# Kernel optimization log

Hardware: AMD Instinct MI355X
Metric: run time of the kernel (lower is better)

## Reference

```python
import jax, jax.numpy as jnp
import numpy as np

N_NODES = 100000
N_EDGES = 1600000
D_IN = 128
D_OUT = 128


def setup_inputs() -> dict:
    key = jax.random.key(0)
    k1, k2, k3 = jax.random.split(key, 3)
    x = jax.random.normal(k1, (N_NODES, D_IN), dtype=jnp.float32)
    edge_index = jax.random.randint(k2, (2, N_EDGES), 0, N_NODES, dtype=jnp.int64)
    # glorot-style init for the lazily-created weight
    scale = jnp.sqrt(6.0 / (D_IN + D_OUT)).astype(jnp.float32)
    weight = jax.random.uniform(k3, (D_IN, D_OUT), dtype=jnp.float32, minval=-1.0, maxval=1.0) * scale
    bias = jnp.zeros((D_OUT,), dtype=jnp.float32)
    return {"x": x, "edge_index": edge_index, "weight": weight, "bias": bias}


def reference(x, edge_index, weight, bias):
    N = x.shape[0]
    row, col = edge_index[0], edge_index[1]
    # add_remaining_self_loops: drop existing self-loops (equivalently zero their
    # weight) and append a self-loop of weight 1.0 for every node (improved=False).
    ew = jnp.where(row == col, 0.0, 1.0).astype(x.dtype)
    loop = jnp.arange(N, dtype=row.dtype)
    row = jnp.concatenate([row, loop])
    col = jnp.concatenate([col, loop])
    ew = jnp.concatenate([ew, jnp.ones((N,), dtype=x.dtype)])
    # degree via scatter-add on destination (col), deg^{-1/2} with inf -> 0
    deg = jax.ops.segment_sum(ew, col, num_segments=N)
    deg_inv_sqrt = jnp.where(deg > 0, jax.lax.rsqrt(deg), 0.0).astype(x.dtype)
    norm = deg_inv_sqrt[row] * ew * deg_inv_sqrt[col]  # [E+N]
    # dense transform then gather-scale-scatter (GCN message passing, aggr='add')
    xw = x @ weight  # [N, D_OUT]
    msgs = norm[:, None] * xw[row]  # [E+N, D_OUT] gather on source nodes
    out = jax.ops.segment_sum(msgs, col, num_segments=N)  # scatter-add to dest
    return out + bias
```

## Files before the change

kernel.cpp:

```cpp
#include <hip/hip_runtime.h>
#include <hip/hip_bf16.h>

#define NN 100000
#define NE 1600000
#define D  128
#define NPAD 100352
#define NBLK 782
#define CAP  64

#define BSH   9
#define NB_C  196
#define CAPB  9216
#define NB_P3 250
#define CHUNK 6400
#define EPT   25

typedef __attribute__((ext_vector_type(8))) short short8;
typedef __attribute__((ext_vector_type(4))) float floatx4;

__device__ __forceinline__ unsigned short f2b(float f) {
    __hip_bfloat16 h = __float2bfloat16(f);
    return *(unsigned short*)&h;
}
__device__ __forceinline__ float b2f(unsigned short u) {
    return __uint_as_float(((unsigned)u) << 16);
}

__global__ __launch_bounds__(256) void k_part(const int* __restrict__ row,
                                              const int* __restrict__ col,
                                              int* __restrict__ bcnt,
                                              unsigned int* __restrict__ edgesP) {
    __shared__ unsigned int  vals[CHUNK];
    __shared__ unsigned short buck[CHUNK];
    __shared__ int hist[NB_C], basep[NB_C], cur[NB_C];
    int t = threadIdx.x;
    size_t e0 = (size_t)blockIdx.x * CHUNK;

    for (int i = t; i < NB_C; i += 256) { hist[i] = 0; cur[i] = 0; }
    __syncthreads();

#pragma unroll
    for (int i = 0; i < EPT; ++i) {
        int idx = i * 256 + t;
        int r = row[e0 + idx], c = col[e0 + idx];
        bool valid = (r != c);
        vals[idx] = (unsigned)r | ((unsigned)(c & 511) << 17);
        buck[idx] = valid ? (unsigned short)(c >> BSH) : (unsigned short)0xFFFF;
        if (valid) atomicAdd(&hist[c >> BSH], 1);
    }
    __syncthreads();

    for (int i = t; i < NB_C; i += 256)
        basep[i] = atomicAdd(&bcnt[i], hist[i]);
    __syncthreads();

#pragma unroll
    for (int i = 0; i < EPT; ++i) {
        int idx = i * 256 + t;
        unsigned short b = buck[idx];
        if (b != 0xFFFF) {
            int rk = atomicAdd(&cur[b], 1);
            int pos = basep[b] + rk;
            if (pos < CAPB) edgesP[(size_t)b * CAPB + pos] = vals[idx];
        }
    }
}

__global__ __launch_bounds__(256) void k_fine(const int* __restrict__ bcnt,
                                              const unsigned int* __restrict__ edgesP,
                                              int* __restrict__ counts,
                                              int* __restrict__ srcs) {
    __shared__ int cnt[512];
    int t = threadIdx.x, b = blockIdx.x;
    int n0 = b << BSH;
    for (int i = t; i < 512; i += 256) cnt[i] = 0;
    __syncthreads();

    int m = min(bcnt[b], CAPB);
    const unsigned int* ep = edgesP + (size_t)b * CAPB;
    for (int i = t; i < m; i += 256) {
        unsigned int v = ep[i];
        int c0 = v >> 17;
        int s  = v & 0x1FFFF;
        int pos = atomicAdd(&cnt[c0], 1);
        if (pos < CAP) srcs[(size_t)(n0 + c0) * CAP + pos] = s;
    }
    __syncthreads();
    for (int i = t; i < 512; i += 256) counts[n0 + i] = cnt[i];
}

__global__ void k_dinv(const int* __restrict__ counts, float* __restrict__ dinv) {
    int i = blockIdx.x * 256 + threadIdx.x;
    if (i < NN) dinv[i] = rsqrtf((float)counts[i] + 1.0f);
}

__global__ void k_prep_w(const float* __restrict__ w, unsigned short* __restrict__ wt) {
    int i = blockIdx.x * 256 + threadIdx.x;
    int n = i >> 7, k = i & 127;
    wt[i] = f2b(w[k * D + n]);
}

__global__ __launch_bounds__(256, 2) void k_gemm_mfma(const float* __restrict__ x,
                                                      const unsigned short* __restrict__ wt,
                                                      const float* __restrict__ dinv,
                                                      unsigned short* __restrict__ yw) {
    __shared__ unsigned short sX[128 * 128];
    __shared__ unsigned short sW[128 * 128];
    __shared__ float sD[128];
    int tid = threadIdx.x;
    long row0 = (long)blockIdx.x * 128;

    if (tid < 128) {
        long gr = row0 + tid;
        sD[tid] = (gr < NN) ? dinv[gr] : 0.0f;
    }
    {
        const uint4* src = (const uint4*)wt;
        uint4* dst = (uint4*)sW;
#pragma unroll
        for (int j = 0; j < 8; ++j) dst[tid + j * 256] = src[tid + j * 256];
    }
#pragma unroll
    for (int j = 0; j < 16; ++j) {
        int i = tid + j * 256;
        int r = i >> 5, q = i & 31;
        float4 v = make_float4(0.f, 0.f, 0.f, 0.f);
        long gr = row0 + r;
        if (gr < NN) v = *(const float4*)(x + gr * D + q * 4);
        ushort4 u;
        u.x = f2b(v.x); u.y = f2b(v.y); u.z = f2b(v.z); u.w = f2b(v.w);
        *(ushort4*)&sX[r * D + q * 4] = u;
    }
    __syncthreads();

    int lane = tid & 63, wave = tid >> 6;
    int wm = (wave & 1) * 64, wn = (wave >> 1) * 64;
    int lrow = lane & 15, lkb = (lane >> 4) * 8;

    floatx4 acc[4][4] = {};
#pragma unroll
    for (int kc = 0; kc < 4; ++kc) {
        int kb = kc * 32 + lkb;
        short8 bfr[4];
#pragma unroll
        for (int tn = 0; tn < 4; ++tn)
            bfr[tn] = *(const short8*)&sW[(wn + tn * 16 + lrow) * D + kb];
#pragma unroll
        for (int tm = 0; tm < 4; ++tm) {
            short8 afr = *(const short8*)&sX[(wm + tm * 16 + lrow) * D + kb];
#pragma unroll
            for (int tn = 0; tn < 4; ++tn)
                acc[tm][tn] = __builtin_amdgcn_mfma_f32_16x16x32_bf16(afr, bfr[tn], acc[tm][tn], 0, 0, 0);
        }
    }

    int orow = (lane >> 4) * 4;
    int ocol = lane & 15;
#pragma unroll
    for (int tm = 0; tm < 4; ++tm) {
#pragma unroll
        for (int reg = 0; reg < 4; ++reg) {
            int  rt = wm + tm * 16 + orow + reg;
            long m  = row0 + rt;
            if (m < NN) {
                float dm = sD[rt];
                unsigned short* o = yw + m * D + wn + ocol;
#pragma unroll
                for (int tn = 0; tn < 4; ++tn) o[tn * 16] = f2b(acc[tm][tn][reg] * dm);
            }
        }
    }
}

__global__ __launch_bounds__(128) void k_agg(const int* __restrict__ counts,
                                             const int* __restrict__ srcs,
                                             const float* __restrict__ dinv,
                                             const unsigned short* __restrict__ yw,
                                             const float* __restrict__ bias,
                                             float* __restrict__ out) {
    int c = blockIdx.x;
    int j = threadIdx.x;
    int cnt = min(counts[c], CAP);
    const int* sp = srcs + (size_t)c * CAP;

    float acc = b2f(yw[(size_t)c * D + j]);

    int p = 0;
    for (; p + 4 <= cnt; p += 4) {
        int s0 = sp[p], s1 = sp[p + 1], s2 = sp[p + 2], s3 = sp[p + 3];
        float x0 = b2f(yw[(size_t)s0 * D + j]);
        float x1 = b2f(yw[(size_t)s1 * D + j]);
        float x2 = b2f(yw[(size_t)s2 * D + j]);
        float x3 = b2f(yw[(size_t)s3 * D + j]);
        acc += x0 + x1 + x2 + x3;
    }
    for (; p < cnt; ++p) acc += b2f(yw[(size_t)sp[p] * D + j]);

    out[(size_t)c * D + j] = dinv[c] * acc + bias[j];
}

extern "C" void kernel_launch(void* const* d_in, const int* in_sizes, int n_in,
                              void* d_out, int out_size, void* d_ws, size_t ws_size,
                              hipStream_t stream) {
    const float* x    = (const float*)d_in[0];
    const int*   ei   = (const int*)d_in[1];
    const float* w    = (const float*)d_in[2];
    const float* bias = (const float*)d_in[3];
    float*       out  = (float*)d_out;

    const int* row = ei;
    const int* col = ei + NE;

    int*   counts = (int*)d_ws;
    float* dinv   = (float*)(counts + NPAD);
    int*   srcs   = (int*)(dinv + NPAD);
    unsigned short* yw = (unsigned short*)(srcs + (size_t)NN * CAP);
    unsigned short* wt = yw + (size_t)NN * D;
    int*   bcnt   = (int*)(wt + 128 * 128);
    unsigned int* edgesP = (unsigned int*)yw;

    hipMemsetAsync(bcnt, 0, NB_C * sizeof(int), stream);

    k_prep_w<<<64, 256, 0, stream>>>(w, wt);
    k_part<<<NB_P3, 256, 0, stream>>>(row, col, bcnt, edgesP);
    k_fine<<<NB_C, 256, 0, stream>>>(bcnt, edgesP, counts, srcs);
    k_dinv <<<(NN + 255) / 256, 256, 0, stream>>>(counts, dinv);
    k_gemm_mfma<<<NBLK, 256, 0, stream>>>(x, wt, dinv, yw);
    k_agg  <<<NN, 128, 0, stream>>>(counts, srcs, dinv, yw, bias, out);
}
```

Measured before the change: 257.8 us.

## Rework partition, fuse dinv into fine pass, and wave-per-node packed aggregation

The partition kernel now uses smaller chunks held in registers across more blocks, and ranks edges in a single atomic pass, dropping the shared staging arrays. The dinv computation moves into the fine bucketing kernel, which removes one launch. Aggregation assigns one wave per destination node. Each lane loads a packed pair of bf16 values, and source indices are loaded once and broadcast with shuffles, with an unroll of 8 for more loads in flight. Together these aim to cut launch count, shared-memory traffic and per-edge index loads, at the cost of more register pressure and more global atomics on bcnt.

New measurement: 242.9 us. 1.06x faster.

```diff
diff --git a/kernel.cpp b/kernel.cpp
--- a/kernel.cpp
+++ b/kernel.cpp
@@ -8,12 +8,12 @@
 #define NBLK 782
 #define CAP  64
 
-#define BSH   9
-#define NB_C  196
-#define CAPB  9216
-#define NB_P3 250
-#define CHUNK 6400
-#define EPT   25
+#define BSH    9
+#define NB_C   196
+#define CAPB   9216
+#define PCHUNK 2048
+#define PEPT   8
+#define NPART  782
 
 typedef __attribute__((ext_vector_type(8))) short short8;
 typedef __attribute__((ext_vector_type(4))) float floatx4;
@@ -30,38 +30,39 @@
                                               const int* __restrict__ col,
                                               int* __restrict__ bcnt,
                                               unsigned int* __restrict__ edgesP) {
-    __shared__ unsigned int  vals[CHUNK];
-    __shared__ unsigned short buck[CHUNK];
-    __shared__ int hist[NB_C], basep[NB_C], cur[NB_C];
+    __shared__ int cur[NB_C], basep[NB_C];
     int t = threadIdx.x;
-    size_t e0 = (size_t)blockIdx.x * CHUNK;
-
-    for (int i = t; i < NB_C; i += 256) { hist[i] = 0; cur[i] = 0; }
-    __syncthreads();
-
-#pragma unroll
-    for (int i = 0; i < EPT; ++i) {
-        int idx = i * 256 + t;
-        int r = row[e0 + idx], c = col[e0 + idx];
-        bool valid = (r != c);
-        vals[idx] = (unsigned)r | ((unsigned)(c & 511) << 17);
-        buck[idx] = valid ? (unsigned short)(c >> BSH) : (unsigned short)0xFFFF;
-        if (valid) atomicAdd(&hist[c >> BSH], 1);
+    size_t e0 = (size_t)blockIdx.x * PCHUNK;
+
+    for (int i = t; i < NB_C; i += 256) cur[i] = 0;
+    __syncthreads();
+
+    unsigned int val[PEPT];
+    int bk[PEPT], rk[PEPT];
+#pragma unroll
+    for (int i = 0; i < PEPT; ++i) {
+        size_t e = e0 + i * 256 + t;
+        bk[i] = -1;
+        if (e < NE) {
+            int r = row[e], c = col[e];
+            if (r != c) {
+                bk[i]  = c >> BSH;
+                val[i] = (unsigned)r | ((unsigned)(c & 511) << 17);
+                rk[i]  = atomicAdd(&cur[bk[i]], 1);
+            }
+        }
     }
     __syncthreads();
 
     for (int i = t; i < NB_C; i += 256)
-        basep[i] = atomicAdd(&bcnt[i], hist[i]);
-    __syncthreads();
-
-#pragma unroll
-    for (int i = 0; i < EPT; ++i) {
-        int idx = i * 256 + t;
-        unsigned short b = buck[idx];
-        if (b != 0xFFFF) {
-            int rk = atomicAdd(&cur[b], 1);
-            int pos = basep[b] + rk;
-            if (pos < CAPB) edgesP[(size_t)b * CAPB + pos] = vals[idx];
+        basep[i] = cur[i] ? atomicAdd(&bcnt[i], cur[i]) : 0;
+    __syncthreads();
+
+#pragma unroll
+    for (int i = 0; i < PEPT; ++i) {
+        if (bk[i] >= 0) {
+            int pos = basep[bk[i]] + rk[i];
+            if (pos < CAPB) edgesP[(size_t)bk[i] * CAPB + pos] = val[i];
         }
     }
 }
@@ -69,6 +70,7 @@
 __global__ __launch_bounds__(256) void k_fine(const int* __restrict__ bcnt,
                                               const unsigned int* __restrict__ edgesP,
                                               int* __restrict__ counts,
+                                              float* __restrict__ dinv,
                                               int* __restrict__ srcs) {
     __shared__ int cnt[512];
     int t = threadIdx.x, b = blockIdx.x;
@@ -86,12 +88,12 @@
         if (pos < CAP) srcs[(size_t)(n0 + c0) * CAP + pos] = s;
     }
     __syncthreads();
-    for (int i = t; i < 512; i += 256) counts[n0 + i] = cnt[i];
-}
-
-__global__ void k_dinv(const int* __restrict__ counts, float* __restrict__ dinv) {
-    int i = blockIdx.x * 256 + threadIdx.x;
-    if (i < NN) dinv[i] = rsqrtf((float)counts[i] + 1.0f);
+    for (int i = t; i < 512; i += 256) {
+        int n = n0 + i;
+        int cv = cnt[i];
+        counts[n] = min(cv, CAP);
+        dinv[n] = rsqrtf((float)cv + 1.0f);
+    }
 }
 
 __global__ void k_prep_w(const float* __restrict__ w, unsigned short* __restrict__ wt) {
@@ -172,31 +174,50 @@
     }
 }
 
-__global__ __launch_bounds__(128) void k_agg(const int* __restrict__ counts,
+__global__ __launch_bounds__(256) void k_agg(const int* __restrict__ counts,
                                              const int* __restrict__ srcs,
                                              const float* __restrict__ dinv,
-                                             const unsigned short* __restrict__ yw,
+                                             const unsigned int* __restrict__ ywp,
                                              const float* __restrict__ bias,
                                              float* __restrict__ out) {
-    int c = blockIdx.x;
-    int j = threadIdx.x;
-    int cnt = min(counts[c], CAP);
+    int lane = threadIdx.x & 63;
+    int c = blockIdx.x * 4 + (threadIdx.x >> 6);
+
+    int cnt = counts[c];
     const int* sp = srcs + (size_t)c * CAP;
-
-    float acc = b2f(yw[(size_t)c * D + j]);
+    int mysrc = (lane < cnt) ? sp[lane] : 0;
+
+    unsigned int u = ywp[(size_t)c * 64 + lane];
+    float acc0 = __uint_as_float(u << 16);
+    float acc1 = __uint_as_float(u & 0xFFFF0000u);
 
     int p = 0;
-    for (; p + 4 <= cnt; p += 4) {
-        int s0 = sp[p], s1 = sp[p + 1], s2 = sp[p + 2], s3 = sp[p + 3];
-        float x0 = b2f(yw[(size_t)s0 * D + j]);
-        float x1 = b2f(yw[(size_t)s1 * D + j]);
-        float x2 = b2f(yw[(size_t)s2 * D + j]);
-        float x3 = b2f(yw[(size_t)s3 * D + j]);
-        acc += x0 + x1 + x2 + x3;
-    }
-    for (; p < cnt; ++p) acc += b2f(yw[(size_t)sp[p] * D + j]);
-
-    out[(size_t)c * D + j] = dinv[c] * acc + bias[j];
+    for (; p + 8 <= cnt; p += 8) {
+        unsigned int v[8];
+#pragma unroll
+        for (int i = 0; i < 8; ++i) {
+            int s = __shfl(mysrc, p + i);
+            v[i] = ywp[(size_t)s * 64 + lane];
+        }
+#pragma unroll
+        for (int i = 0; i < 8; ++i) {
+            acc0 += __uint_as_float(v[i] << 16);
+            acc1 += __uint_as_float(v[i] & 0xFFFF0000u);
+        }
+    }
+    for (; p < cnt; ++p) {
+        int s = __shfl(mysrc, p);
+        unsigned int v = ywp[(size_t)s * 64 + lane];
+        acc0 += __uint_as_float(v << 16);
+        acc1 += __uint_as_float(v & 0xFFFF0000u);
+    }
+
+    float dc = dinv[c];
+    float2 b2 = ((const float2*)bias)[lane];
+    float2 o;
+    o.x = dc * acc0 + b2.x;
+    o.y = dc * acc1 + b2.y;
+    ((float2*)(out + (size_t)c * D))[lane] = o;
 }
 
 extern "C" void kernel_launch(void* const* d_in, const int* in_sizes, int n_in,
@@ -222,9 +243,8 @@
     hipMemsetAsync(bcnt, 0, NB_C * sizeof(int), stream);
 
     k_prep_w<<<64, 256, 0, stream>>>(w, wt);
-    k_part<<<NB_P3, 256, 0, stream>>>(row, col, bcnt, edgesP);
-    k_fine<<<NB_C, 256, 0, stream>>>(bcnt, edgesP, counts, srcs);
-    k_dinv <<<(NN + 255) / 256, 256, 0, stream>>>(counts, dinv);
+    k_part<<<NPART, 256, 0, stream>>>(row, col, bcnt, edgesP);
+    k_fine<<<NB_C, 256, 0, stream>>>(bcnt, edgesP, counts, dinv, srcs);
     k_gemm_mfma<<<NBLK, 256, 0, stream>>>(x, wt, dinv, yw);
-    k_agg  <<<NN, 128, 0, stream>>>(counts, srcs, dinv, yw, bias, out);
-}
+    k_agg<<<NN / 4, 256, 0, stream>>>(counts, srcs, dinv, (const unsigned int*)yw, bias, out);
+}
```
